# Kernel optimization log

Hardware: AMD Instinct MI355X
Metric: run time of the kernel (lower is better)

The kernel has to match this reference:

```python
import jax, jax.numpy as jnp
import numpy as np

EPS = 1e-12  # F.normalize eps


def _l2_normalize(x):
    n = jnp.sqrt(jnp.sum(x * x, axis=1, keepdims=True))
    return x / jnp.maximum(n, EPS)


def setup_inputs() -> dict:
    key = jax.random.key(0)
    k1, k2, k3 = jax.random.split(key, 3)
    N, B, D = 1024, 1024, 128
    return {
        "node_embedding": jax.random.normal(k1, (N, D), dtype=jnp.float32),
        "graph_embedding": jax.random.normal(k2, (B, D), dtype=jnp.float32),
        "graph_metric": jax.random.uniform(k3, (B, B), dtype=jnp.float32),
    }


def reference(node_embedding, graph_embedding, graph_metric):
    # L2 normalize (F.normalize p=2 dim=1)
    ne = _l2_normalize(node_embedding)   # [N, D]
    ge = _l2_normalize(graph_embedding)  # [B, D]
    N, D = ne.shape

    # pairwise concatenated embeddings: replaces the O(N^2) python loop of
    # torch.cat((ne[i], ne[j])) + stack with one broadcast-and-concat pass.
    left = jnp.broadcast_to(ne[:, None, :], (N, N, D))
    right = jnp.broadcast_to(ne[None, :, :], (N, N, D))
    pairwise_embeddings_matrix = jnp.concatenate([left, right], axis=-1).reshape(N * N, 2 * D)

    # node loss: 'CL' branch — cross entropy with identity soft labels.
    node_logits = ne @ ne.T  # [N, N]
    # -mean over rows of sum(eye * log_softmax) == -mean(diag(log_softmax))
    node_logp = jax.nn.log_softmax(node_logits, axis=1)
    node_loss = -jnp.mean(jnp.diagonal(node_logp))

    # graph loss: else branch — genGraphMetric ends with row softmax.
    gm = jax.nn.softmax(graph_metric, axis=-1)  # [B, B]
    graph_logits = ge @ ge.T                    # [B, B]
    lp = jax.nn.log_softmax(graph_logits, axis=1)
    lpT = jax.nn.log_softmax(graph_logits.T, axis=1)
    graph_loss = (-jnp.mean(jnp.sum(gm * lp, axis=1))
                  - jnp.mean(jnp.sum(gm.T * lpT, axis=1)))

    alpha = 0.5
    loss = alpha * node_loss + (1.0 - alpha) * graph_loss
    return (loss, node_loss, graph_loss, graph_logits, pairwise_embeddings_matrix)
```

## Files before the change

kernel.cpp:

```cpp
#include <hip/hip_runtime.h>
#include <math.h>

#define NN 1024
#define DD 128
#define BB 1024
#define TI 8
#define TJ 32

typedef float floatx4 __attribute__((ext_vector_type(4)));

__device__ __forceinline__ float waveReduceSum(float v) {
#pragma unroll
  for (int off = 32; off > 0; off >>= 1) v += __shfl_xor(v, off);
  return v;
}
__device__ __forceinline__ float waveReduceMax(float v) {
#pragma unroll
  for (int off = 32; off > 0; off >>= 1) v = fmaxf(v, __shfl_xor(v, off));
  return v;
}

__global__ __launch_bounds__(64) void prep_kernel(
    const float* __restrict__ ne, const float* __restrict__ ge,
    const float* __restrict__ gm, float* __restrict__ ne_n,
    float* __restrict__ ge_n, float* __restrict__ gm_max,
    float* __restrict__ gm_den) {
  int b = blockIdx.x;
  int lane = threadIdx.x;
  if (b < NN + BB) {
    const float* src;
    float* dst;
    if (b < NN) { src = ne + (size_t)b * DD; dst = ne_n + (size_t)b * DD; }
    else { src = ge + (size_t)(b - NN) * DD; dst = ge_n + (size_t)(b - NN) * DD; }
    float2 v = ((const float2*)src)[lane];
    float ss = v.x * v.x + v.y * v.y;
    ss = waveReduceSum(ss);
    float scale = 1.0f / fmaxf(sqrtf(ss), 1e-12f);
    float2 o;
    o.x = v.x * scale;
    o.y = v.y * scale;
    ((float2*)dst)[lane] = o;
  } else {
    int row = b - (NN + BB);
    const float4* r = (const float4*)(gm + (size_t)row * BB);
    float vals[16];
    float m = -INFINITY;
#pragma unroll
    for (int k = 0; k < 4; ++k) {
      float4 v = r[lane + 64 * k];
      vals[k * 4 + 0] = v.x; vals[k * 4 + 1] = v.y;
      vals[k * 4 + 2] = v.z; vals[k * 4 + 3] = v.w;
      m = fmaxf(m, fmaxf(fmaxf(v.x, v.y), fmaxf(v.z, v.w)));
    }
    m = waveReduceMax(m);
    float s = 0.f;
#pragma unroll
    for (int t = 0; t < 16; ++t) s += expf(vals[t] - m);
    s = waveReduceSum(s);
    if (lane == 0) { gm_max[row] = m; gm_den[row] = s; }
  }
}

__global__ __launch_bounds__(256) void loss_kernel(
    const float* __restrict__ nen, const float* __restrict__ gen,
    const float* __restrict__ gm, const float* __restrict__ gm_max,
    const float* __restrict__ gm_den, float* __restrict__ out_logits,
    float* __restrict__ node_partial, float* __restrict__ graph_partial) {
  int bid = blockIdx.x;
  int tid = threadIdx.x;
  int lane = tid & 63, wid = tid >> 6;
  int g = lane >> 4, gl = lane & 15;
  __shared__ float q[DD];
  __shared__ float logits[NN];
  __shared__ float red[8];

  if (bid < 1024) {
    int i = bid;
    if (tid < DD) q[tid] = nen[(size_t)i * DD + tid];
    __syncthreads();
    const float4* qv = (const float4*)q;
    float4 b0 = qv[gl * 2], b1 = qv[gl * 2 + 1];
#pragma unroll 4
    for (int p = 0; p < 64; ++p) {
      int j = p * 16 + wid * 4 + g;
      const float4* rowp = (const float4*)(nen + (size_t)j * DD);
      float4 a0 = rowp[gl * 2], a1 = rowp[gl * 2 + 1];
      float acc = a0.x * b0.x + a0.y * b0.y + a0.z * b0.z + a0.w * b0.w +
                  a1.x * b1.x + a1.y * b1.y + a1.z * b1.z + a1.w * b1.w;
      acc += __shfl_xor(acc, 1);
      acc += __shfl_xor(acc, 2);
      acc += __shfl_xor(acc, 4);
      acc += __shfl_xor(acc, 8);
      if (gl == 0) logits[j] = acc;
    }
    __syncthreads();
    float lv[4];
    float m = -INFINITY;
#pragma unroll
    for (int k = 0; k < 4; ++k) {
      lv[k] = logits[tid + 256 * k];
      m = fmaxf(m, lv[k]);
    }
    m = waveReduceMax(m);
    if (lane == 0) red[wid] = m;
    __syncthreads();
    float M = fmaxf(fmaxf(red[0], red[1]), fmaxf(red[2], red[3]));
    float s = 0.f;
#pragma unroll
    for (int k = 0; k < 4; ++k) s += expf(lv[k] - M);
    s = waveReduceSum(s);
    if (lane == 0) red[4 + wid] = s;
    __syncthreads();
    float S = red[4] + red[5] + red[6] + red[7];
    if (tid == 0) node_partial[i] = logits[i] - (M + logf(S));
  } else {
    int i = bid - 1024;
    if (tid < DD) q[tid] = gen[(size_t)i * DD + tid];
    __syncthreads();
    const float4* qv = (const float4*)q;
    float4 b0 = qv[gl * 2], b1 = qv[gl * 2 + 1];
#pragma unroll 4
    for (int p = 0; p < 64; ++p) {
      int j = p * 16 + wid * 4 + g;
      const float4* rowp = (const float4*)(gen + (size_t)j * DD);
      float4 a0 = rowp[gl * 2], a1 = rowp[gl * 2 + 1];
      float acc = a0.x * b0.x + a0.y * b0.y + a0.z * b0.z + a0.w * b0.w +
                  a1.x * b1.x + a1.y * b1.y + a1.z * b1.z + a1.w * b1.w;
      acc += __shfl_xor(acc, 1);
      acc += __shfl_xor(acc, 2);
      acc += __shfl_xor(acc, 4);
      acc += __shfl_xor(acc, 8);
      if (gl == 0) logits[j] = acc;
    }
    __syncthreads();
    float lv[4];
    float m = -INFINITY;
#pragma unroll
    for (int k = 0; k < 4; ++k) {
      lv[k] = logits[tid + 256 * k];
      m = fmaxf(m, lv[k]);
      out_logits[(size_t)i * BB + tid + 256 * k] = lv[k];
    }
    m = waveReduceMax(m);
    if (lane == 0) red[wid] = m;
    __syncthreads();
    float M = fmaxf(fmaxf(red[0], red[1]), fmaxf(red[2], red[3]));
    float s = 0.f;
#pragma unroll
    for (int k = 0; k < 4; ++k) s += expf(lv[k] - M);
    s = waveReduceSum(s);
    if (lane == 0) red[4 + wid] = s;
    __syncthreads();
    float S = red[4] + red[5] + red[6] + red[7];
    float lse = M + logf(S);
    float gmx_i = gm_max[i];
    float inv_i = 1.0f / gm_den[i];
    float c = 0.f;
#pragma unroll
    for (int k = 0; k < 4; ++k) {
      int j = tid + 256 * k;
      float lp = lv[k] - lse;
      float wij = expf(gm[(size_t)i * BB + j] - gmx_i) * inv_i;
      float wji = expf(gm[(size_t)j * BB + i] - gm_max[j]) / gm_den[j];
      c += (wij + wji) * lp;
    }
    c = waveReduceSum(c);
    __syncthreads();
    if (lane == 0) red[wid] = c;
    __syncthreads();
    if (tid == 0) graph_partial[i] = red[0] + red[1] + red[2] + red[3];
  }
}

__global__ __launch_bounds__(256) void pairwise_kernel(
    const float* __restrict__ nen, float* __restrict__ outp) {
  int b = blockIdx.x;
  int bi = b >> 5, bj = b & 31;
  int I0 = bi * TI, J0 = bj * TJ;
  int tid = threadIdx.x;
  int lane = tid & 63;
  int w = tid >> 6;

  __shared__ float SHI[TI][DD];
  __shared__ float SHJ[TJ][DD];
  __shared__ float LJ0[TJ];
  __shared__ float LI0[TI];
  __shared__ float LI0N[TI];

#pragma unroll
  for (int p = 0; p < 5; ++p) {
    int task = tid + 256 * p;
    int row = task >> 5;
    int c4 = task & 31;
    const float* src = (row < TI) ? nen + (size_t)(I0 + row) * DD
                                  : nen + (size_t)(J0 + row - TI) * DD;
    floatx4 A = *(const floatx4*)(src + 4 * c4);
    float nxt = __shfl_down(A.x, 1);
    floatx4 Sv;
    Sv.x = A.y; Sv.y = A.z; Sv.z = A.w; Sv.w = nxt;
    float* dst = (row < TI) ? &SHI[row][4 * c4] : &SHJ[row - TI][4 * c4];
    *(floatx4*)dst = Sv;
    if (c4 == 0) {
      if (row < TI) {
        LI0[row] = A.x;
        int nr = I0 + row + 1;
        if (nr > 1023) nr = 0;
        LI0N[row] = nen[(size_t)nr * DD];
      } else {
        LJ0[row - TI] = A.x;
      }
    }
  }
  __syncthreads();

  bool is31 = (lane == 31);
  bool is63 = (lane == 63);
  bool patch = is31 | is63;
  bool lastSeg = (bj == 31) && (w == 3);
  bool tailThread = (b == 4095) && (tid == 255);

  for (int ic = 0; ic < TI; ++ic) {
    float li0 = LI0[ic];
    float li0n = LI0N[ic];
    size_t segf = (((size_t)(I0 + ic) << 10) + (size_t)J0) << 8;
    float* gb = outp + segf + 1 + 4 * tid;
#pragma unroll
    for (int q = 0; q < 8; ++q) {
      int jc = w + 4 * q;
      const float* addr = (lane < 32) ? &SHI[ic][4 * lane]
                                      : &SHJ[jc][4 * (lane - 32)];
      floatx4 v = *(const floatx4*)addr;
      float lj0 = LJ0[jc];
      float spec = is31 ? lj0 : ((lastSeg && q == 7) ? li0n : li0);
      v.w = patch ? spec : v.w;
      if (tailThread && ic == TI - 1 && q == 7) {
        gb[0] = v.x; gb[1] = v.y; gb[2] = v.z;
      } else {
        *(floatx4*)gb = v;
      }
      gb += 1024;
    }
  }
  if (b == 0 && tid == 0) outp[0] = nen[0];
}

__global__ __launch_bounds__(256) void final_kernel(
    const float* __restrict__ node_partial,
    const float* __restrict__ graph_partial, float* __restrict__ out) {
  int tid = threadIdx.x;
  int lane = tid & 63, wid = tid >> 6;
  __shared__ float red[8];
  float ns = 0.f, gs = 0.f;
#pragma unroll
  for (int k = 0; k < 4; ++k) {
    ns += node_partial[tid + 256 * k];
    gs += graph_partial[tid + 256 * k];
  }
  ns = waveReduceSum(ns);
  gs = waveReduceSum(gs);
  if (lane == 0) { red[wid] = ns; red[4 + wid] = gs; }
  __syncthreads();
  if (tid == 0) {
    float nsum = red[0] + red[1] + red[2] + red[3];
    float gsum = red[4] + red[5] + red[6] + red[7];
    float node_loss = -nsum / (float)NN;
    float graph_loss = -gsum / (float)BB;
    float loss = 0.5f * node_loss + 0.5f * graph_loss;
    out[0] = loss;
    out[1] = node_loss;
    out[2] = graph_loss;
  }
}

extern "C" void kernel_launch(void* const* d_in, const int* in_sizes, int n_in,
                              void* d_out, int out_size, void* d_ws,
                              size_t ws_size, hipStream_t stream) {
  const float* ne = (const float*)d_in[0];
  const float* ge = (const float*)d_in[1];
  const float* gm = (const float*)d_in[2];
  float* out = (float*)d_out;
  float* ws = (float*)d_ws;

  float* ne_n = ws;
  float* ge_n = ws + 131072;
  float* gm_max = ws + 262144;
  float* gm_den = ws + 263168;
  float* node_partial = ws + 264192;
  float* graph_partial = ws + 265216;

  float* out_logits = out + 3;
  float* out_pair = out + 3 + (size_t)NN * NN;

  hipLaunchKernelGGL(prep_kernel, dim3(NN + 2 * BB), dim3(64), 0, stream,
                     ne, ge, gm, ne_n, ge_n, gm_max, gm_den);
  hipLaunchKernelGGL(loss_kernel, dim3(2048), dim3(256), 0, stream,
                     ne_n, ge_n, gm, gm_max, gm_den, out_logits,
                     node_partial, graph_partial);
  hipLaunchKernelGGL(pairwise_kernel, dim3(4096), dim3(256), 0, stream,
                     ne_n, out_pair);
  hipLaunchKernelGGL(final_kernel, dim3(1), dim3(256), 0, stream,
                     node_partial, graph_partial, out);
}
```

Measured before the change: 271.6 us.

## Fuse loss and pairwise kernels into one interleaved grid

Merges the compute-bound loss kernel and the store-bound pairwise-concat kernel into a single launch of 6144 blocks. Blocks are interleaved 2:1 (two pairwise blocks per loss block) so memory-heavy writes overlap with the dot-product and softmax work. This also removes one kernel launch and its tail. In exchange, shared memory is sized for the larger path, which may lower occupancy for the loss blocks.

```diff
diff --git a/kernel.cpp b/kernel.cpp
--- a/kernel.cpp
+++ b/kernel.cpp
@@ -61,28 +61,102 @@
   }
 }
 
-__global__ __launch_bounds__(256) void loss_kernel(
+__global__ __launch_bounds__(256) void fused_kernel(
     const float* __restrict__ nen, const float* __restrict__ gen,
     const float* __restrict__ gm, const float* __restrict__ gm_max,
     const float* __restrict__ gm_den, float* __restrict__ out_logits,
-    float* __restrict__ node_partial, float* __restrict__ graph_partial) {
-  int bid = blockIdx.x;
+    float* __restrict__ outp, float* __restrict__ node_partial,
+    float* __restrict__ graph_partial) {
+  __shared__ __align__(16) char smem[20672];
+  int b = blockIdx.x;
   int tid = threadIdx.x;
-  int lane = tid & 63, wid = tid >> 6;
+  int lane = tid & 63;
+  int w = tid >> 6;
+  int m3 = b % 3;
+
+  if (m3 != 2) {
+    int pwId = (b / 3) * 2 + m3;
+    int bi = pwId >> 5, bj = pwId & 31;
+    int I0 = bi * TI, J0 = bj * TJ;
+    float (*SHI)[DD] = (float (*)[DD])smem;
+    float (*SHJ)[DD] = (float (*)[DD])(smem + 4096);
+    float* LJ0 = (float*)(smem + 20480);
+    float* LI0 = (float*)(smem + 20608);
+    float* LI0N = (float*)(smem + 20640);
+
+#pragma unroll
+    for (int p = 0; p < 5; ++p) {
+      int task = tid + 256 * p;
+      int row = task >> 5;
+      int c4 = task & 31;
+      const float* src = (row < TI) ? nen + (size_t)(I0 + row) * DD
+                                    : nen + (size_t)(J0 + row - TI) * DD;
+      floatx4 A = *(const floatx4*)(src + 4 * c4);
+      float nxt = __shfl_down(A.x, 1);
+      floatx4 Sv;
+      Sv.x = A.y; Sv.y = A.z; Sv.z = A.w; Sv.w = nxt;
+      float* dst = (row < TI) ? &SHI[row][4 * c4] : &SHJ[row - TI][4 * c4];
+      *(floatx4*)dst = Sv;
+      if (c4 == 0) {
+        if (row < TI) {
+          LI0[row] = A.x;
+          int nr = I0 + row + 1;
+          if (nr > 1023) nr = 0;
+          LI0N[row] = nen[(size_t)nr * DD];
+        } else {
+          LJ0[row - TI] = A.x;
+        }
+      }
+    }
+    __syncthreads();
+
+    bool is31 = (lane == 31);
+    bool is63 = (lane == 63);
+    bool patch = is31 | is63;
+    bool lastSeg = (bj == 31) && (w == 3);
+    bool tailThread = (pwId == 4095) && (tid == 255);
+
+    for (int ic = 0; ic < TI; ++ic) {
+      float li0 = LI0[ic];
+      float li0n = LI0N[ic];
+      size_t segf = (((size_t)(I0 + ic) << 10) + (size_t)J0) << 8;
+      float* gb = outp + segf + 1 + 4 * tid;
+#pragma unroll
+      for (int q = 0; q < 8; ++q) {
+        int jc = w + 4 * q;
+        const float* addr = (lane < 32) ? &SHI[ic][4 * lane]
+                                        : &SHJ[jc][4 * (lane - 32)];
+        floatx4 v = *(const floatx4*)addr;
+        float lj0 = LJ0[jc];
+        float spec = is31 ? lj0 : ((lastSeg && q == 7) ? li0n : li0);
+        v.w = patch ? spec : v.w;
+        if (tailThread && ic == TI - 1 && q == 7) {
+          gb[0] = v.x; gb[1] = v.y; gb[2] = v.z;
+        } else {
+          *(floatx4*)gb = v;
+        }
+        gb += 1024;
+      }
+    }
+    if (pwId == 0 && tid == 0) outp[0] = nen[0];
+    return;
+  }
+
+  int lossId = b / 3;
+  float* q = (float*)smem;
+  float* logits = q + DD;
+  float* red = logits + NN;
   int g = lane >> 4, gl = lane & 15;
-  __shared__ float q[DD];
-  __shared__ float logits[NN];
-  __shared__ float red[8];
-
-  if (bid < 1024) {
-    int i = bid;
+
+  if (lossId < 1024) {
+    int i = lossId;
     if (tid < DD) q[tid] = nen[(size_t)i * DD + tid];
     __syncthreads();
     const float4* qv = (const float4*)q;
     float4 b0 = qv[gl * 2], b1 = qv[gl * 2 + 1];
 #pragma unroll 4
     for (int p = 0; p < 64; ++p) {
-      int j = p * 16 + wid * 4 + g;
+      int j = p * 16 + w * 4 + g;
       const float4* rowp = (const float4*)(nen + (size_t)j * DD);
       float4 a0 = rowp[gl * 2], a1 = rowp[gl * 2 + 1];
       float acc = a0.x * b0.x + a0.y * b0.y + a0.z * b0.z + a0.w * b0.w +
@@ -102,26 +176,26 @@
       m = fmaxf(m, lv[k]);
     }
     m = waveReduceMax(m);
-    if (lane == 0) red[wid] = m;
+    if (lane == 0) red[w] = m;
     __syncthreads();
     float M = fmaxf(fmaxf(red[0], red[1]), fmaxf(red[2], red[3]));
     float s = 0.f;
 #pragma unroll
     for (int k = 0; k < 4; ++k) s += expf(lv[k] - M);
     s = waveReduceSum(s);
-    if (lane == 0) red[4 + wid] = s;
+    if (lane == 0) red[4 + w] = s;
     __syncthreads();
     float S = red[4] + red[5] + red[6] + red[7];
     if (tid == 0) node_partial[i] = logits[i] - (M + logf(S));
   } else {
-    int i = bid - 1024;
+    int i = lossId - 1024;
     if (tid < DD) q[tid] = gen[(size_t)i * DD + tid];
     __syncthreads();
     const float4* qv = (const float4*)q;
     float4 b0 = qv[gl * 2], b1 = qv[gl * 2 + 1];
 #pragma unroll 4
     for (int p = 0; p < 64; ++p) {
-      int j = p * 16 + wid * 4 + g;
+      int j = p * 16 + w * 4 + g;
       const float4* rowp = (const float4*)(gen + (size_t)j * DD);
       float4 a0 = rowp[gl * 2], a1 = rowp[gl * 2 + 1];
       float acc = a0.x * b0.x + a0.y * b0.y + a0.z * b0.z + a0.w * b0.w +
@@ -142,14 +216,14 @@
       out_logits[(size_t)i * BB + tid + 256 * k] = lv[k];
     }
     m = waveReduceMax(m);
-    if (lane == 0) red[wid] = m;
+    if (lane == 0) red[w] = m;
     __syncthreads();
     float M = fmaxf(fmaxf(red[0], red[1]), fmaxf(red[2], red[3]));
     float s = 0.f;
 #pragma unroll
     for (int k = 0; k < 4; ++k) s += expf(lv[k] - M);
     s = waveReduceSum(s);
-    if (lane == 0) red[4 + wid] = s;
+    if (lane == 0) red[4 + w] = s;
     __syncthreads();
     float S = red[4] + red[5] + red[6] + red[7];
     float lse = M + logf(S);
@@ -166,82 +240,10 @@
     }
     c = waveReduceSum(c);
     __syncthreads();
-    if (lane == 0) red[wid] = c;
+    if (lane == 0) red[w] = c;
     __syncthreads();
     if (tid == 0) graph_partial[i] = red[0] + red[1] + red[2] + red[3];
   }
-}
-
-__global__ __launch_bounds__(256) void pairwise_kernel(
-    const float* __restrict__ nen, float* __restrict__ outp) {
-  int b = blockIdx.x;
-  int bi = b >> 5, bj = b & 31;
-  int I0 = bi * TI, J0 = bj * TJ;
-  int tid = threadIdx.x;
-  int lane = tid & 63;
-  int w = tid >> 6;
-
-  __shared__ float SHI[TI][DD];
-  __shared__ float SHJ[TJ][DD];
-  __shared__ float LJ0[TJ];
-  __shared__ float LI0[TI];
-  __shared__ float LI0N[TI];
-
-#pragma unroll
-  for (int p = 0; p < 5; ++p) {
-    int task = tid + 256 * p;
-    int row = task >> 5;
-    int c4 = task & 31;
-    const float* src = (row < TI) ? nen + (size_t)(I0 + row) * DD
-                                  : nen + (size_t)(J0 + row - TI) * DD;
-    floatx4 A = *(const floatx4*)(src + 4 * c4);
-    float nxt = __shfl_down(A.x, 1);
-    floatx4 Sv;
-    Sv.x = A.y; Sv.y = A.z; Sv.z = A.w; Sv.w = nxt;
-    float* dst = (row < TI) ? &SHI[row][4 * c4] : &SHJ[row - TI][4 * c4];
-    *(floatx4*)dst = Sv;
-    if (c4 == 0) {
-      if (row < TI) {
-        LI0[row] = A.x;
-        int nr = I0 + row + 1;
-        if (nr > 1023) nr = 0;
-        LI0N[row] = nen[(size_t)nr * DD];
-      } else {
-        LJ0[row - TI] = A.x;
-      }
-    }
-  }
-  __syncthreads();
-
-  bool is31 = (lane == 31);
-  bool is63 = (lane == 63);
-  bool patch = is31 | is63;
-  bool lastSeg = (bj == 31) && (w == 3);
-  bool tailThread = (b == 4095) && (tid == 255);
-
-  for (int ic = 0; ic < TI; ++ic) {
-    float li0 = LI0[ic];
-    float li0n = LI0N[ic];
-    size_t segf = (((size_t)(I0 + ic) << 10) + (size_t)J0) << 8;
-    float* gb = outp + segf + 1 + 4 * tid;
-#pragma unroll
-    for (int q = 0; q < 8; ++q) {
-      int jc = w + 4 * q;
-      const float* addr = (lane < 32) ? &SHI[ic][4 * lane]
-                                      : &SHJ[jc][4 * (lane - 32)];
-      floatx4 v = *(const floatx4*)addr;
-      float lj0 = LJ0[jc];
-      float spec = is31 ? lj0 : ((lastSeg && q == 7) ? li0n : li0);
-      v.w = patch ? spec : v.w;
-      if (tailThread && ic == TI - 1 && q == 7) {
-        gb[0] = v.x; gb[1] = v.y; gb[2] = v.z;
-      } else {
-        *(floatx4*)gb = v;
-      }
-      gb += 1024;
-    }
-  }
-  if (b == 0 && tid == 0) outp[0] = nen[0];
 }
 
 __global__ __launch_bounds__(256) void final_kernel(
@@ -293,11 +295,9 @@
 
   hipLaunchKernelGGL(prep_kernel, dim3(NN + 2 * BB), dim3(64), 0, stream,
                      ne, ge, gm, ne_n, ge_n, gm_max, gm_den);
-  hipLaunchKernelGGL(loss_kernel, dim3(2048), dim3(256), 0, stream,
+  hipLaunchKernelGGL(fused_kernel, dim3(6144), dim3(256), 0, stream,
                      ne_n, ge_n, gm, gm_max, gm_den, out_logits,
-                     node_partial, graph_partial);
-  hipLaunchKernelGGL(pairwise_kernel, dim3(4096), dim3(256), 0, stream,
-                     ne_n, out_pair);
+                     out_pair, node_partial, graph_partial);
   hipLaunchKernelGGL(final_kernel, dim3(1), dim3(256), 0, stream,
                      node_partial, graph_partial, out);
 }
```

After: 242.3 us. 1.12x faster.
